# Optimization experiments

Measured on AMD Instinct MI355X. Metric: run time of the kernel, lower is better.

The kernel has to match this reference:

```python
import jax, jax.numpy as jnp
import numpy as np

N = 100000
E = 3200000
IN_FEATS = 128
HID_FEATS = 128
OUT_FEATS = 128
MLP_HID = 128
MLP_OUT = 64


def setup_inputs() -> dict:
    key = jax.random.key(0)
    ks = jax.random.split(key, 12)
    x = jax.random.normal(ks[0], (N, IN_FEATS), dtype=jnp.float32)
    src = jax.random.randint(ks[1], (E,), 0, N, dtype=jnp.int32)
    dst = jax.random.randint(ks[2], (E,), 0, N, dtype=jnp.int32)
    s = 0.05
    W1 = jax.random.normal(ks[3], (IN_FEATS, HID_FEATS), dtype=jnp.float32) * s
    b1 = jnp.zeros((HID_FEATS,), dtype=jnp.float32)
    W2 = jax.random.normal(ks[4], (HID_FEATS, OUT_FEATS), dtype=jnp.float32) * s
    b2 = jnp.zeros((OUT_FEATS,), dtype=jnp.float32)
    Wm1 = jax.random.normal(ks[5], (OUT_FEATS, MLP_HID), dtype=jnp.float32) * s
    bm1 = jnp.zeros((MLP_HID,), dtype=jnp.float32)
    Wm2 = jax.random.normal(ks[6], (MLP_HID, MLP_OUT), dtype=jnp.float32) * s
    bm2 = jnp.zeros((MLP_OUT,), dtype=jnp.float32)
    return {"x": x, "src": src, "dst": dst, "W1": W1, "b1": b1,
            "W2": W2, "b2": b2, "Wm1": Wm1, "bm1": bm1, "Wm2": Wm2, "bm2": bm2}


def _graph_conv(h, src, dst, W, b, out_norm, in_norm):
    # DGL GraphConv norm='both': rst = D_in^{-1/2} * A^T (D_out^{-1/2} * h) @ W + b
    msg = (h * out_norm[:, None])[src]                       # [E, F] gather
    agg = jax.ops.segment_sum(msg, dst, num_segments=N)      # [N, F] scatter-add
    return (agg * in_norm[:, None]) @ W + b


def _forward(x, src, dst, W1, b1, W2, b2, Wm1, bm1, Wm2, bm2):
    ones = jnp.ones((src.shape[0],), dtype=x.dtype)
    out_deg = jnp.maximum(jax.ops.segment_sum(ones, src, num_segments=N), 1.0)
    in_deg = jnp.maximum(jax.ops.segment_sum(ones, dst, num_segments=N), 1.0)
    out_norm = out_deg ** -0.5
    in_norm = in_deg ** -0.5
    # conv1 + ReLU (dropout identity in eval mode)
    h = jax.nn.relu(_graph_conv(x, src, dst, W1, b1, out_norm, in_norm))
    # conv2 + ReLU
    h = jax.nn.relu(_graph_conv(h, src, dst, W2, b2, out_norm, in_norm))
    # MLP head: Linear -> ReLU -> Linear -> sigmoid (act='sigmoid')
    h = jax.nn.relu(h @ Wm1 + bm1)
    h = jax.nn.sigmoid(h @ Wm2 + bm2)
    return h


def reference(x, src, dst, W1, b1, W2, b2, Wm1, bm1, Wm2, bm2):
    return _forward(x, src, dst, W1, b1, W2, b2, Wm1, bm1, Wm2, bm2)
```

## Files before the change

### kernel.cpp

```cpp
#include <hip/hip_runtime.h>
#include <math.h>

#define NNODES 100000
#define NEDGES 3200000
#define F 128
#define NPB 512
#define NB ((NNODES + NPB - 1) / NPB)
#define CAP 20480
#define T2 8192

typedef __attribute__((ext_vector_type(8))) short short8;
typedef __attribute__((ext_vector_type(4))) float f32x4;

__device__ __forceinline__ unsigned short f2bf(float f) {
    unsigned u = __float_as_uint(f);
    unsigned r = u + 0x7fff + ((u >> 16) & 1);
    return (unsigned short)(r >> 16);
}
__device__ __forceinline__ float bflo(unsigned u) { return __uint_as_float(u << 16); }
__device__ __forceinline__ float bfhi(unsigned u) { return __uint_as_float(u & 0xffff0000u); }


__global__ void init_cursors_kernel(int* __restrict__ dcur, int* __restrict__ scur) {
    int b = blockIdx.x * 256 + threadIdx.x;
    if (b < NB) { dcur[b] = b * CAP; scur[b] = b * CAP; }
}


__global__ __launch_bounds__(256) void dual_bin_kernel(const int* __restrict__ src,
                                                       const int* __restrict__ dst,
                                                       int* __restrict__ dcur,
                                                       int* __restrict__ scur,
                                                       unsigned* __restrict__ epk,
                                                       unsigned short* __restrict__ esl) {
    __shared__ unsigned pk[T2];
    __shared__ unsigned short sl[T2];
    __shared__ unsigned char db[T2], sb[T2];
    __shared__ int dh[NB], dbase[NB], dlc[NB];
    __shared__ int sh[NB], sbase[NB], slc[NB];
    int t = threadIdx.x;
    for (int i = t; i < NB; i += 256) { dh[i] = 0; dlc[i] = 0; sh[i] = 0; slc[i] = 0; }
    __syncthreads();
    int e0 = blockIdx.x * T2;
    int n = min(T2, NEDGES - e0);
    for (int i = t; i < n; i += 256) {
        int s = src[e0 + i], d = dst[e0 + i];
        int bd = d >> 9, bs = s >> 9;
        pk[i] = (unsigned)s | ((unsigned)(d & 511) << 17);
        sl[i] = (unsigned short)(s & 511);
        db[i] = (unsigned char)bd;
        sb[i] = (unsigned char)bs;
        atomicAdd(&dh[bd], 1);
        atomicAdd(&sh[bs], 1);
    }
    __syncthreads();
    for (int b = t; b < NB; b += 256) {
        if (dh[b]) dbase[b] = atomicAdd(&dcur[b], dh[b]);
        if (sh[b]) sbase[b] = atomicAdd(&scur[b], sh[b]);
    }
    __syncthreads();
    for (int i = t; i < n; i += 256) {
        int b = db[i];
        epk[dbase[b] + atomicAdd(&dlc[b], 1)] = pk[i];
    }
    for (int i = t; i < n; i += 256) {
        int b = sb[i];
        esl[sbase[b] + atomicAdd(&slc[b], 1)] = sl[i];
    }
}


__global__ __launch_bounds__(512) void src_hist_kernel(const unsigned short* __restrict__ esl,
                                                       const int* __restrict__ scur,
                                                       float* __restrict__ out_norm) {
    __shared__ int cnt[NPB];
    int t = threadIdx.x, b = blockIdx.x;
    cnt[t] = 0;
    __syncthreads();
    int e0 = b * CAP, e1 = scur[b];
    for (int i = e0 + t; i < e1; i += 512) atomicAdd(&cnt[esl[i]], 1);
    __syncthreads();
    int node = b * NPB + t;
    if (node < NNODES) out_norm[node] = rsqrtf((float)max(cnt[t], 1));
}


__global__ __launch_bounds__(512) void bucket_csr_kernel(const unsigned* __restrict__ epk,
                                                         const int* __restrict__ dcur,
                                                         int2* __restrict__ row_span,
                                                         float* __restrict__ in_norm,
                                                         int* __restrict__ csr_src) {
    __shared__ int hist[NPB], off[NPB], lcur[NPB];
    int t = threadIdx.x, b = blockIdx.x;
    hist[t] = 0; lcur[t] = 0;
    __syncthreads();
    int e0 = b * CAP, e1 = dcur[b];
    for (int i = e0 + t; i < e1; i += 512)
        atomicAdd(&hist[epk[i] >> 17], 1);
    __syncthreads();
    int h = hist[t];
    off[t] = h;
    __syncthreads();
    for (int d = 1; d < NPB; d <<= 1) {
        int u = (t >= d) ? off[t - d] : 0;
        __syncthreads();
        off[t] += u;
        __syncthreads();
    }
    int excl = off[t] - h;
    int node = b * NPB + t;
    if (node < NNODES) {
        row_span[node] = make_int2(e0 + excl, e0 + excl + h);
        in_norm[node] = rsqrtf((float)max(h, 1));
    }
    __syncthreads();
    off[t] = excl;
    __syncthreads();
    for (int i = e0 + t; i < e1; i += 512) {
        unsigned p = epk[i];
        int dl = p >> 17;
        csr_src[e0 + off[dl] + atomicAdd(&lcur[dl], 1)] = (int)(p & 0x1FFFF);
    }
}


__global__ __launch_bounds__(256) void scale_to_bf16_kernel(const float* __restrict__ x,
                                                            const float* __restrict__ out_norm,
                                                            uint2* __restrict__ hs) {
    int tid = blockIdx.x * 256 + threadIdx.x;
    if (tid >= NNODES * 32) return;
    int row = tid >> 5, q = tid & 31;
    float nrm = out_norm[row];
    float4 v = *(const float4*)(x + (size_t)row * F + q * 4);
    uint2 o;
    o.x = (unsigned)f2bf(v.x * nrm) | ((unsigned)f2bf(v.y * nrm) << 16);
    o.y = (unsigned)f2bf(v.z * nrm) | ((unsigned)f2bf(v.w * nrm) << 16);
    hs[(size_t)row * 32 + q] = o;
}


__global__ void pack_all_kernel(const float* __restrict__ W1, const float* __restrict__ W2,
                                const float* __restrict__ Wm1, const float* __restrict__ Wm2,
                                short8* __restrict__ Wp) {
    int idx = blockIdx.x * 256 + threadIdx.x;
    if (idx >= 7168) return;
    const float* W; int ncol, base;
    if (idx < 2048)      { W = W1;  ncol = 128; base = 0; }
    else if (idx < 4096) { W = W2;  ncol = 128; base = 2048; }
    else if (idx < 6144) { W = Wm1; ncol = 128; base = 4096; }
    else                 { W = Wm2; ncol = 64;  base = 6144; }
    int li = idx - base;
    int lane = li & 63, s = (li >> 6) & 3, c = li >> 8;
    int nn = c * 16 + (lane & 15);
    int k0 = s * 32 + (lane >> 4) * 8;
    short8 v;
#pragma unroll
    for (int j = 0; j < 8; j++) v[j] = (short)f2bf(W[(size_t)(k0 + j) * ncol + nn]);
    Wp[idx] = v;
}


__global__ __launch_bounds__(256) void aggregate_kernel(const unsigned* __restrict__ hs,
                                                        const int2* __restrict__ row_span,
                                                        const int* __restrict__ csr_src,
                                                        const float* __restrict__ in_norm,
                                                        unsigned* __restrict__ outv) {
    int wave = threadIdx.x >> 6;
    int lane = threadIdx.x & 63;
    int node = blockIdx.x * 4 + wave;
    if (node >= NNODES) return;
    int2 sp = row_span[node];
    int beg = sp.x, end = sp.y;
    float ax = 0.f, ay = 0.f;
    int j = beg;
    for (; j + 8 <= end; j += 8) {
        int s0 = csr_src[j],     s1 = csr_src[j + 1], s2 = csr_src[j + 2], s3 = csr_src[j + 3];
        int s4 = csr_src[j + 4], s5 = csr_src[j + 5], s6 = csr_src[j + 6], s7 = csr_src[j + 7];
        unsigned u0 = hs[(size_t)s0 * 64 + lane];
        unsigned u1 = hs[(size_t)s1 * 64 + lane];
        unsigned u2 = hs[(size_t)s2 * 64 + lane];
        unsigned u3 = hs[(size_t)s3 * 64 + lane];
        unsigned u4 = hs[(size_t)s4 * 64 + lane];
        unsigned u5 = hs[(size_t)s5 * 64 + lane];
        unsigned u6 = hs[(size_t)s6 * 64 + lane];
        unsigned u7 = hs[(size_t)s7 * 64 + lane];
        ax += bflo(u0) + bflo(u1) + bflo(u2) + bflo(u3)
            + bflo(u4) + bflo(u5) + bflo(u6) + bflo(u7);
        ay += bfhi(u0) + bfhi(u1) + bfhi(u2) + bfhi(u3)
            + bfhi(u4) + bfhi(u5) + bfhi(u6) + bfhi(u7);
    }
    for (; j < end; j++) {
        unsigned u0 = hs[(size_t)csr_src[j] * 64 + lane];
        ax += bflo(u0);
        ay += bfhi(u0);
    }
    float inn = in_norm[node];
    outv[(size_t)node * 64 + lane] =
        (unsigned)f2bf(ax * inn) | ((unsigned)f2bf(ay * inn) << 16);
}


template <int SCALE>
__global__ __launch_bounds__(256) void gemm_mfma_kernel(const unsigned short* __restrict__ A,
                                                        const short8* __restrict__ Bp,
                                                        const float* __restrict__ bias,
                                                        const float* __restrict__ out_norm,
                                                        unsigned short* __restrict__ Cout, int nrows) {
    int w = threadIdx.x >> 6, lane = threadIdx.x & 63;
    int m = lane & 15, quad = lane >> 4;
    int row0 = blockIdx.x * 64 + w * 16;

    int arow = min(row0 + m, nrows - 1);
    short8 afrag[4];
#pragma unroll
    for (int s = 0; s < 4; s++)
        afrag[s] = *(const short8*)(A + (size_t)arow * F + s * 32 + quad * 8);

    int baseRow = row0 + quad * 4;
    float nrm[4];
    if (SCALE) {
#pragma unroll
        for (int r = 0; r < 4; r++) nrm[r] = out_norm[min(baseRow + r, nrows - 1)];
    }

#pragma unroll
    for (int c = 0; c < 8; c++) {
        f32x4 acc = {0.f, 0.f, 0.f, 0.f};
#pragma unroll
        for (int s = 0; s < 4; s++) {
            short8 b = Bp[(c * 4 + s) * 64 + lane];
            acc = __builtin_amdgcn_mfma_f32_16x16x32_bf16(afrag[s], b, acc, 0, 0, 0);
        }
        float bc = bias[c * 16 + m];
#pragma unroll
        for (int r = 0; r < 4; r++) {
            int row = baseRow + r;
            if (row < nrows) {
                float v = fmaxf(acc[r] + bc, 0.f);
                if (SCALE) v *= nrm[r];
                Cout[(size_t)row * F + c * 16 + m] = f2bf(v);
            }
        }
    }
}


__global__ __launch_bounds__(256) void mlp_fused_kernel(const unsigned short* __restrict__ A,
                                                        const short8* __restrict__ Bp1,
                                                        const float* __restrict__ bm1,
                                                        const short8* __restrict__ Bp2,
                                                        const float* __restrict__ bm2,
                                                        float* __restrict__ out, int nrows) {
    __shared__ unsigned short h3[4][16][136];
    int w = threadIdx.x >> 6, lane = threadIdx.x & 63;
    int m = lane & 15, quad = lane >> 4;
    int row0 = blockIdx.x * 64 + w * 16;

    int arow = min(row0 + m, nrows - 1);
    short8 afrag[4];
#pragma unroll
    for (int s = 0; s < 4; s++)
        afrag[s] = *(const short8*)(A + (size_t)arow * F + s * 32 + quad * 8);

#pragma unroll
    for (int c = 0; c < 8; c++) {
        f32x4 acc = {0.f, 0.f, 0.f, 0.f};
#pragma unroll
        for (int s = 0; s < 4; s++) {
            short8 b = Bp1[(c * 4 + s) * 64 + lane];
            acc = __builtin_amdgcn_mfma_f32_16x16x32_bf16(afrag[s], b, acc, 0, 0, 0);
        }
        float bc = bm1[c * 16 + m];
#pragma unroll
        for (int r = 0; r < 4; r++)
            h3[w][quad * 4 + r][c * 16 + m] = f2bf(fmaxf(acc[r] + bc, 0.f));
    }
    __syncthreads();

    short8 a2[4];
#pragma unroll
    for (int s = 0; s < 4; s++)
        a2[s] = *(const short8*)(&h3[w][m][s * 32 + quad * 8]);

    int baseRow = row0 + quad * 4;
#pragma unroll
    for (int c2 = 0; c2 < 4; c2++) {
        f32x4 acc = {0.f, 0.f, 0.f, 0.f};
#pragma unroll
        for (int s = 0; s < 4; s++) {
            short8 b = Bp2[(c2 * 4 + s) * 64 + lane];
            acc = __builtin_amdgcn_mfma_f32_16x16x32_bf16(a2[s], b, acc, 0, 0, 0);
        }
        float bc = bm2[c2 * 16 + m];
#pragma unroll
        for (int r = 0; r < 4; r++) {
            int row = baseRow + r;
            if (row < nrows)
                out[(size_t)row * 64 + c2 * 16 + m] = 1.f / (1.f + __expf(-(acc[r] + bc)));
        }
    }
}


extern "C" void kernel_launch(void* const* d_in, const int* in_sizes, int n_in,
                              void* d_out, int out_size, void* d_ws, size_t ws_size,
                              hipStream_t stream) {
    const float* x   = (const float*)d_in[0];
    const int* src   = (const int*)d_in[1];
    const int* dst   = (const int*)d_in[2];
    const float* W1  = (const float*)d_in[3];
    const float* b1  = (const float*)d_in[4];
    const float* W2  = (const float*)d_in[5];
    const float* b2  = (const float*)d_in[6];
    const float* Wm1 = (const float*)d_in[7];
    const float* bm1 = (const float*)d_in[8];
    const float* Wm2 = (const float*)d_in[9];
    const float* bm2 = (const float*)d_in[10];
    float* out = (float*)d_out;

    char* w = (char*)d_ws;
    int* dcur          = (int*)w;   w += (size_t)(NB + 4) * 4;
    int* scur          = (int*)w;   w += (size_t)(NB + 4) * 4;
    float* out_norm    = (float*)w; w += (size_t)NNODES * 4;
    float* in_norm     = (float*)w; w += (size_t)NNODES * 4;
    int2* row_span     = (int2*)w;  w += (size_t)NNODES * 8;
    int* csr_src       = (int*)w;   w += (size_t)NB * CAP * 4;
    unsigned* epk      = (unsigned*)w; w += (size_t)NB * CAP * 4;
    unsigned short* esl= (unsigned short*)w; w += (size_t)NB * CAP * 2;
    short8* Wp         = (short8*)w; w += (size_t)7168 * 16;
    unsigned* bufX     = (unsigned*)w; w += (size_t)NNODES * 64 * 4;
    unsigned* bufY     = (unsigned*)w; w += (size_t)NNODES * 64 * 4;

    init_cursors_kernel<<<1, 256, 0, stream>>>(dcur, scur);
    dual_bin_kernel<<<(NEDGES + T2 - 1) / T2, 256, 0, stream>>>(src, dst, dcur, scur, epk, esl);
    src_hist_kernel<<<NB, 512, 0, stream>>>(esl, scur, out_norm);
    bucket_csr_kernel<<<NB, 512, 0, stream>>>(epk, dcur, row_span, in_norm, csr_src);
    scale_to_bf16_kernel<<<(NNODES * 32 + 255) / 256, 256, 0, stream>>>(x, out_norm, (uint2*)bufX);
    pack_all_kernel<<<28, 256, 0, stream>>>(W1, W2, Wm1, Wm2, Wp);

    const int aggGrid = (NNODES + 3) / 4;
    const int gemmGrid = (NNODES + 63) / 64;

    aggregate_kernel<<<aggGrid, 256, 0, stream>>>(bufX, row_span, csr_src, in_norm, bufY);
    gemm_mfma_kernel<1><<<gemmGrid, 256, 0, stream>>>((const unsigned short*)bufY, Wp, b1, out_norm,
                                                      (unsigned short*)bufX, NNODES);
    aggregate_kernel<<<aggGrid, 256, 0, stream>>>(bufX, row_span, csr_src, in_norm, bufY);
    gemm_mfma_kernel<0><<<gemmGrid, 256, 0, stream>>>((const unsigned short*)bufY, Wp + 2048, b2, out_norm,
                                                      (unsigned short*)bufX, NNODES);
    mlp_fused_kernel<<<gemmGrid, 256, 0, stream>>>((const unsigned short*)bufX, Wp + 4096, bm1,
                                                   Wp + 6144, bm2, out, NNODES);
}
```

Before: 567.6 us.

## Slice node features into 16-column panels for cache-local aggregation

Stores the bf16 feature matrices as 8 column slices of 16 features each, laid out slice-major, and runs aggregation over a 2D grid with one slice per grid row. Each wave handles 8 edges at a time with 8 lanes per 32-byte row, then reduces across lanes with shuffles. The aim is to make each slice's gather working set (about 3.2 MB) small enough to stay in cache and to put more gathers in flight per wave. The trade-off is extra shuffle reductions, redundant CSR index reads per slice, and the GEMM having to read and write in the sliced layout.

```diff
diff --git a/kernel.cpp b/kernel.cpp
--- a/kernel.cpp
+++ b/kernel.cpp
@@ -124,18 +124,17 @@
 }
 
 
-__global__ __launch_bounds__(256) void scale_to_bf16_kernel(const float* __restrict__ x,
-                                                            const float* __restrict__ out_norm,
-                                                            uint2* __restrict__ hs) {
+__global__ __launch_bounds__(256) void scale_slice_kernel(const float* __restrict__ x,
+                                                          const float* __restrict__ out_norm,
+                                                          unsigned* __restrict__ hsS) {
     int tid = blockIdx.x * 256 + threadIdx.x;
-    if (tid >= NNODES * 32) return;
-    int row = tid >> 5, q = tid & 31;
+    if (tid >= NNODES * 64) return;
+    int row = tid >> 6, l = tid & 63;
+    int s = l >> 3, q = l & 7;
     float nrm = out_norm[row];
-    float4 v = *(const float4*)(x + (size_t)row * F + q * 4);
-    uint2 o;
-    o.x = (unsigned)f2bf(v.x * nrm) | ((unsigned)f2bf(v.y * nrm) << 16);
-    o.y = (unsigned)f2bf(v.z * nrm) | ((unsigned)f2bf(v.w * nrm) << 16);
-    hs[(size_t)row * 32 + q] = o;
+    float2 v = *(const float2*)(x + (size_t)row * F + 2 * l);
+    hsS[((size_t)s * NNODES + row) * 8 + q] =
+        (unsigned)f2bf(v.x * nrm) | ((unsigned)f2bf(v.y * nrm) << 16);
 }
 
 
@@ -160,47 +159,43 @@
 }
 
 
-__global__ __launch_bounds__(256) void aggregate_kernel(const unsigned* __restrict__ hs,
-                                                        const int2* __restrict__ row_span,
-                                                        const int* __restrict__ csr_src,
-                                                        const float* __restrict__ in_norm,
-                                                        unsigned* __restrict__ outv) {
+__global__ __launch_bounds__(256) void aggregate_slice_kernel(const unsigned* __restrict__ hsS,
+                                                              const int2* __restrict__ row_span,
+                                                              const int* __restrict__ csr_src,
+                                                              const float* __restrict__ in_norm,
+                                                              unsigned* __restrict__ outS) {
     int wave = threadIdx.x >> 6;
     int lane = threadIdx.x & 63;
+    int g = lane >> 3, q = lane & 7;
     int node = blockIdx.x * 4 + wave;
-    if (node >= NNODES) return;
+    int s = blockIdx.y;
+    const unsigned* hs = hsS + (size_t)s * NNODES * 8;
     int2 sp = row_span[node];
     int beg = sp.x, end = sp.y;
-    float ax = 0.f, ay = 0.f;
-    int j = beg;
-    for (; j + 8 <= end; j += 8) {
-        int s0 = csr_src[j],     s1 = csr_src[j + 1], s2 = csr_src[j + 2], s3 = csr_src[j + 3];
-        int s4 = csr_src[j + 4], s5 = csr_src[j + 5], s6 = csr_src[j + 6], s7 = csr_src[j + 7];
-        unsigned u0 = hs[(size_t)s0 * 64 + lane];
-        unsigned u1 = hs[(size_t)s1 * 64 + lane];
-        unsigned u2 = hs[(size_t)s2 * 64 + lane];
-        unsigned u3 = hs[(size_t)s3 * 64 + lane];
-        unsigned u4 = hs[(size_t)s4 * 64 + lane];
-        unsigned u5 = hs[(size_t)s5 * 64 + lane];
-        unsigned u6 = hs[(size_t)s6 * 64 + lane];
-        unsigned u7 = hs[(size_t)s7 * 64 + lane];
-        ax += bflo(u0) + bflo(u1) + bflo(u2) + bflo(u3)
-            + bflo(u4) + bflo(u5) + bflo(u6) + bflo(u7);
-        ay += bfhi(u0) + bfhi(u1) + bfhi(u2) + bfhi(u3)
-            + bfhi(u4) + bfhi(u5) + bfhi(u6) + bfhi(u7);
-    }
-    for (; j < end; j++) {
-        unsigned u0 = hs[(size_t)csr_src[j] * 64 + lane];
-        ax += bflo(u0);
-        ay += bfhi(u0);
-    }
-    float inn = in_norm[node];
-    outv[(size_t)node * 64 + lane] =
-        (unsigned)f2bf(ax * inn) | ((unsigned)f2bf(ay * inn) << 16);
-}
-
-
-template <int SCALE>
+    float a0 = 0.f, a1 = 0.f;
+    for (int j = beg; j < end; j += 32) {
+#pragma unroll
+        for (int t = 0; t < 4; t++) {
+            int idx = j + t * 8 + g;
+            int sidx = csr_src[min(idx, end - 1)];
+            unsigned u = hs[(size_t)sidx * 8 + q];
+            if (idx >= end) u = 0u;
+            a0 += bflo(u);
+            a1 += bfhi(u);
+        }
+    }
+    a0 += __shfl_xor(a0, 8);  a1 += __shfl_xor(a1, 8);
+    a0 += __shfl_xor(a0, 16); a1 += __shfl_xor(a1, 16);
+    a0 += __shfl_xor(a0, 32); a1 += __shfl_xor(a1, 32);
+    if (lane < 8) {
+        float inn = in_norm[node];
+        outS[((size_t)s * NNODES + node) * 8 + lane] =
+            (unsigned)f2bf(a0 * inn) | ((unsigned)f2bf(a1 * inn) << 16);
+    }
+}
+
+
+template <int SCALE, int CSLICE>
 __global__ __launch_bounds__(256) void gemm_mfma_kernel(const unsigned short* __restrict__ A,
                                                         const short8* __restrict__ Bp,
                                                         const float* __restrict__ bias,
@@ -213,8 +208,11 @@
     int arow = min(row0 + m, nrows - 1);
     short8 afrag[4];
 #pragma unroll
-    for (int s = 0; s < 4; s++)
-        afrag[s] = *(const short8*)(A + (size_t)arow * F + s * 32 + quad * 8);
+    for (int s = 0; s < 4; s++) {
+        int sl = 2 * s + (quad >> 1);
+        int off = (quad & 1) * 8;
+        afrag[s] = *(const short8*)(A + ((size_t)sl * NNODES + arow) * 16 + off);
+    }
 
     int baseRow = row0 + quad * 4;
     float nrm[4];
@@ -238,7 +236,10 @@
             if (row < nrows) {
                 float v = fmaxf(acc[r] + bc, 0.f);
                 if (SCALE) v *= nrm[r];
-                Cout[(size_t)row * F + c * 16 + m] = f2bf(v);
+                if (CSLICE)
+                    Cout[((size_t)c * NNODES + row) * 16 + m] = f2bf(v);
+                else
+                    Cout[(size_t)row * F + c * 16 + m] = f2bf(v);
             }
         }
     }
@@ -335,18 +336,18 @@
     dual_bin_kernel<<<(NEDGES + T2 - 1) / T2, 256, 0, stream>>>(src, dst, dcur, scur, epk, esl);
     src_hist_kernel<<<NB, 512, 0, stream>>>(esl, scur, out_norm);
     bucket_csr_kernel<<<NB, 512, 0, stream>>>(epk, dcur, row_span, in_norm, csr_src);
-    scale_to_bf16_kernel<<<(NNODES * 32 + 255) / 256, 256, 0, stream>>>(x, out_norm, (uint2*)bufX);
+    scale_slice_kernel<<<(NNODES * 64 + 255) / 256, 256, 0, stream>>>(x, out_norm, bufX);
     pack_all_kernel<<<28, 256, 0, stream>>>(W1, W2, Wm1, Wm2, Wp);
 
-    const int aggGrid = (NNODES + 3) / 4;
+    const dim3 aggGrid(NNODES / 4, 8);
     const int gemmGrid = (NNODES + 63) / 64;
 
-    aggregate_kernel<<<aggGrid, 256, 0, stream>>>(bufX, row_span, csr_src, in_norm, bufY);
-    gemm_mfma_kernel<1><<<gemmGrid, 256, 0, stream>>>((const unsigned short*)bufY, Wp, b1, out_norm,
-                                                      (unsigned short*)bufX, NNODES);
-    aggregate_kernel<<<aggGrid, 256, 0, stream>>>(bufX, row_span, csr_src, in_norm, bufY);
-    gemm_mfma_kernel<0><<<gemmGrid, 256, 0, stream>>>((const unsigned short*)bufY, Wp + 2048, b2, out_norm,
-                                                      (unsigned short*)bufX, NNODES);
+    aggregate_slice_kernel<<<aggGrid, 256, 0, stream>>>(bufX, row_span, csr_src, in_norm, bufY);
+    gemm_mfma_kernel<1, 1><<<gemmGrid, 256, 0, stream>>>((const unsigned short*)bufY, Wp, b1, out_norm,
+                                                         (unsigned short*)bufX, NNODES);
+    aggregate_slice_kernel<<<aggGrid, 256, 0, stream>>>(bufX, row_span, csr_src, in_norm, bufY);
+    gemm_mfma_kernel<0, 0><<<gemmGrid, 256, 0, stream>>>((const unsigned short*)bufY, Wp + 2048, b2, out_norm,
+                                                         (unsigned short*)bufX, NNODES);
     mlp_fused_kernel<<<gemmGrid, 256, 0, stream>>>((const unsigned short*)bufX, Wp + 4096, bm1,
                                                    Wp + 6144, bm2, out, NNODES);
 }
```

Result: slower. 742.0 us (+30.7%).
